# Kernel optimization log

Hardware: AMD Instinct MI355X
Metric: run time of the kernel (lower is better)

Reference implementation:

```python
import jax, jax.numpy as jnp
import numpy as np

B, S, H, NH = 1, 4096, 2048, 16
HD = H // NH
SCALE = HD ** -0.5


def setup_inputs() -> dict:
    key = jax.random.key(0)
    ks = jax.random.split(key, 9)
    std = 1.0 / np.sqrt(H)
    return {
        "hidden_states": jax.random.normal(ks[0], (B, S, H), dtype=jnp.float32),
        "Wq": jax.random.normal(ks[1], (H, H), dtype=jnp.float32) * std,
        "bq": jax.random.normal(ks[2], (H,), dtype=jnp.float32) * std,
        "Wk": jax.random.normal(ks[3], (H, H), dtype=jnp.float32) * std,
        "bk": jax.random.normal(ks[4], (H,), dtype=jnp.float32) * std,
        "Wv": jax.random.normal(ks[5], (H, H), dtype=jnp.float32) * std,
        "bv": jax.random.normal(ks[6], (H,), dtype=jnp.float32) * std,
        "Wo": jax.random.normal(ks[7], (H, H), dtype=jnp.float32) * std,
        "bo": jax.random.normal(ks[8], (H,), dtype=jnp.float32) * std,
    }


def reference(hidden_states, Wq, bq, Wk, bk, Wv, bv, Wo, bo):
    b, s, _ = hidden_states.shape
    # torch nn.Linear: x @ W.T + b
    q = hidden_states @ Wq.T + bq
    k = hidden_states @ Wk.T + bk
    v = hidden_states @ Wv.T + bv
    # [b, nh, s, hd]
    q = q.reshape(b, s, NH, HD).transpose(0, 2, 1, 3)
    k = k.reshape(b, s, NH, HD).transpose(0, 2, 1, 3)
    v = v.reshape(b, s, NH, HD).transpose(0, 2, 1, 3)
    # chunked attention over queries with no mask == full attention
    scores = jnp.einsum('bhqd,bhkd->bhqk', q, k) * SCALE
    attn = jax.nn.softmax(scores, axis=-1)
    out = jnp.einsum('bhqk,bhkd->bhqd', attn, v)
    out = out.transpose(0, 2, 1, 3).reshape(b, s, H)
    return out @ Wo.T + bo
```

## Files before the change

### kernel.cpp

```cpp
#include <hip/hip_runtime.h>
#include <hip/hip_bf16.h>
#include <stdint.h>

#define S_LEN 4096
#define HDIM 2048
#define NHEADS 16
#define HEADDIM 128
#define SCALE_F 0.08838834764831845f
#define MFIX 12.0f

typedef __attribute__((ext_vector_type(8))) short short8;
typedef __attribute__((ext_vector_type(4))) short short4v;
typedef __attribute__((ext_vector_type(4))) float floatx4;
typedef __hip_bfloat16 bf16;

__device__ inline short f2bf(float x) {
  __hip_bfloat16 h = __float2bfloat16(x);
  short s;
  __builtin_memcpy(&s, &h, 2);
  return s;
}

__device__ inline short8 load8_bf16(const float* p) {
  float4 f0 = *(const float4*)p;
  float4 f1 = *(const float4*)(p + 4);
  short8 v;
  v[0] = f2bf(f0.x); v[1] = f2bf(f0.y); v[2] = f2bf(f0.z); v[3] = f2bf(f0.w);
  v[4] = f2bf(f1.x); v[5] = f2bf(f1.y); v[6] = f2bf(f1.z); v[7] = f2bf(f1.w);
  return v;
}
__device__ inline short8 load8_bf16(const bf16* p) { return *(const short8*)p; }

__device__ inline void storeC(bf16* C, size_t idx, float v) { C[idx] = __float2bfloat16(v); }
__device__ inline void storeC(float* C, size_t idx, float v) { C[idx] = v; }

__device__ inline void async_cp16(const void* g, void* l) {
  __builtin_amdgcn_global_load_lds((const __attribute__((address_space(1))) void*)g,
                                   (__attribute__((address_space(3))) void*)l, 16, 0, 0);
}

__global__ __launch_bounds__(256)
void cvt_f32_bf16(const float* __restrict__ in, bf16* __restrict__ out) {
  size_t i = ((size_t)blockIdx.x * 256 + threadIdx.x) * 8;
  *(short8*)((short*)out + i) = load8_bf16(in + i);
}

template<int M, int N, int K, bool TRANSC, bool AASYNC, bool BASYNC,
         typename TA, typename TB, typename TC>
__global__ __launch_bounds__(256, 2)
void gemm_bt(const TA* __restrict__ A, const TB* __restrict__ W,
             const float* __restrict__ bias, TC* __restrict__ C) {
  __shared__ __align__(16) short As[128 * 64];
  __shared__ __align__(16) short Bs[128 * 64];
  const int bn = blockIdx.x * 128;
  const int bm = blockIdx.y * 128;
  const int tid = threadIdx.x;
  const int lane = tid & 63;
  const int wave = tid >> 6;
  const int wr = (wave >> 1) * 64;
  const int wc = (wave & 1) * 64;
  const int ln15 = lane & 15;
  const int quad = lane >> 4;
  const int l8 = lane >> 3;
  const int s8 = lane & 7;
  const int cg = s8 ^ l8;

  floatx4 acc[4][4];
#pragma unroll
  for (int i = 0; i < 4; i++)
#pragma unroll
    for (int j = 0; j < 4; j++) acc[i][j] = floatx4{0.f, 0.f, 0.f, 0.f};

  const TA* Abase = A + (size_t)bm * K;
  const TB* Wbase = W + (size_t)bn * K;

  for (int k0 = 0; k0 < K; k0 += 64) {
#pragma unroll
    for (int is = 0; is < 4; is++) {
      int r = is * 32 + wave * 8 + l8;
      if constexpr (AASYNC)
        async_cp16(Abase + (size_t)r * K + k0 + cg * 8, &As[(is * 32 + wave * 8) * 64]);
      else
        *(short8*)&As[r * 64 + s8 * 8] = load8_bf16(Abase + (size_t)r * K + k0 + cg * 8);
      if constexpr (BASYNC)
        async_cp16(Wbase + (size_t)r * K + k0 + cg * 8, &Bs[(is * 32 + wave * 8) * 64]);
      else
        *(short8*)&Bs[r * 64 + s8 * 8] = load8_bf16(Wbase + (size_t)r * K + k0 + cg * 8);
    }
    __syncthreads();
#pragma unroll
    for (int ks = 0; ks < 2; ks++) {
      short8 af[4], bfr[4];
#pragma unroll
      for (int i = 0; i < 4; i++) {
        int row = wr + i * 16 + ln15;
        af[i] = *(const short8*)&As[row * 64 + (((ks * 4 + quad) ^ (ln15 & 7)) * 8)];
      }
#pragma unroll
      for (int j = 0; j < 4; j++) {
        int row = wc + j * 16 + ln15;
        bfr[j] = *(const short8*)&Bs[row * 64 + (((ks * 4 + quad) ^ (ln15 & 7)) * 8)];
      }
#pragma unroll
      for (int i = 0; i < 4; i++)
#pragma unroll
        for (int j = 0; j < 4; j++)
          acc[i][j] = __builtin_amdgcn_mfma_f32_16x16x32_bf16(af[i], bfr[j], acc[i][j], 0, 0, 0);
    }
    __syncthreads();
  }
#pragma unroll
  for (int j = 0; j < 4; j++) {
    int col = bn + wc + j * 16 + ln15;
    float bv = bias[col];
#pragma unroll
    for (int i = 0; i < 4; i++) {
      int row0 = bm + wr + i * 16 + quad * 4;
      if constexpr (TRANSC) {
        short4v v;
#pragma unroll
        for (int r = 0; r < 4; r++) v[r] = f2bf(acc[i][j][r] + bv);
        *(short4v*)&C[(size_t)col * M + row0] = v;
      } else {
#pragma unroll
        for (int r = 0; r < 4; r++)
          storeC(C, (size_t)(row0 + r) * N + col, acc[i][j][r] + bv);
      }
    }
  }
}

__global__ __launch_bounds__(256, 2)
void flash_attn(const bf16* Qg, const bf16* __restrict__ Kg,
                const bf16* __restrict__ VTg, bf16* Og) {
  __shared__ __align__(16) short Ks[64 * 128];
  __shared__ __align__(16) short Vt[128 * 64];
  __shared__ __align__(16) short Ps[4][32 * 72];

  const int h = blockIdx.x;
  const int q0 = blockIdx.y * 128;
  const int tid = threadIdx.x;
  const int lane = tid & 63;
  const int wave = tid >> 6;
  const int ln15 = lane & 15;
  const int quad = lane >> 4;
  const int l8 = lane >> 3, s8 = lane & 7;
  const int l16 = lane >> 4, s16 = lane & 15;
  const int hoff = h * HEADDIM;
  const int qrow = q0 + wave * 32;

  short8 qf[2][4];
#pragma unroll
  for (int mt = 0; mt < 2; mt++)
#pragma unroll
    for (int ks = 0; ks < 4; ks++)
      qf[mt][ks] = *(const short8*)&Qg[(size_t)(qrow + mt * 16 + ln15) * HDIM + hoff +
                                       ks * 32 + quad * 8];

  floatx4 acc_o[2][8];
#pragma unroll
  for (int mt = 0; mt < 2; mt++)
#pragma unroll
    for (int n = 0; n < 8; n++) acc_o[mt][n] = floatx4{0.f, 0.f, 0.f, 0.f};
  floatx4 l_acc[2] = {floatx4{0.f, 0.f, 0.f, 0.f}, floatx4{0.f, 0.f, 0.f, 0.f}};

  short8 ones;
#pragma unroll
  for (int j = 0; j < 8; j++) ones[j] = (short)0x3F80;

  short* Pw = &Ps[wave][0];

  for (int kv0 = 0; kv0 < S_LEN; kv0 += 64) {
#pragma unroll
    for (int is = 0; is < 4; is++) {
      int r = wave * 16 + is * 4 + l16;
      int cgk = s16 ^ (r & 7);
      async_cp16(&Kg[(size_t)(kv0 + r) * HDIM + hoff + cgk * 8],
                 &Ks[(wave * 16 + is * 4) * 128]);
    }
#pragma unroll
    for (int is = 0; is < 4; is++) {
      int r = wave * 32 + is * 8 + l8;
      async_cp16(&VTg[(size_t)(hoff + r) * S_LEN + kv0 + ((s8 ^ l8) * 8)],
                 &Vt[(wave * 32 + is * 8) * 64]);
    }
    __syncthreads();

    floatx4 sacc[2][4];
#pragma unroll
    for (int mt = 0; mt < 2; mt++)
#pragma unroll
      for (int t = 0; t < 4; t++) sacc[mt][t] = floatx4{0.f, 0.f, 0.f, 0.f};
#pragma unroll
    for (int t = 0; t < 4; t++)
#pragma unroll
      for (int ks = 0; ks < 4; ks++) {
        short8 kf = *(const short8*)&Ks[(t * 16 + ln15) * 128 +
                                        (((ks * 4 + quad) ^ (ln15 & 7)) * 8)];
        sacc[0][t] = __builtin_amdgcn_mfma_f32_16x16x32_bf16(qf[0][ks], kf, sacc[0][t], 0, 0, 0);
        sacc[1][t] = __builtin_amdgcn_mfma_f32_16x16x32_bf16(qf[1][ks], kf, sacc[1][t], 0, 0, 0);
      }

#pragma unroll
    for (int mt = 0; mt < 2; mt++)
#pragma unroll
      for (int t = 0; t < 4; t++)
#pragma unroll
        for (int r = 0; r < 4; r++) {
          float p = __expf(fmaf(sacc[mt][t][r], SCALE_F, -MFIX));
          Pw[(mt * 16 + quad * 4 + r) * 72 + t * 16 + ln15] = f2bf(p);
        }

    short8 pf[2][2];
#pragma unroll
    for (int mt = 0; mt < 2; mt++)
#pragma unroll
      for (int ks = 0; ks < 2; ks++)
        pf[mt][ks] = *(const short8*)&Pw[(mt * 16 + ln15) * 72 + ks * 32 + quad * 8];

#pragma unroll
    for (int mt = 0; mt < 2; mt++)
#pragma unroll
      for (int ks = 0; ks < 2; ks++)
        l_acc[mt] = __builtin_amdgcn_mfma_f32_16x16x32_bf16(pf[mt][ks], ones, l_acc[mt], 0, 0, 0);

#pragma unroll
    for (int n = 0; n < 8; n++)
#pragma unroll
      for (int ks = 0; ks < 2; ks++) {
        short8 vf = *(const short8*)&Vt[(n * 16 + ln15) * 64 +
                                        (((ks * 4 + quad) ^ (ln15 & 7)) * 8)];
        acc_o[0][n] = __builtin_amdgcn_mfma_f32_16x16x32_bf16(pf[0][ks], vf, acc_o[0][n], 0, 0, 0);
        acc_o[1][n] = __builtin_amdgcn_mfma_f32_16x16x32_bf16(pf[1][ks], vf, acc_o[1][n], 0, 0, 0);
      }
    __syncthreads();
  }

#pragma unroll
  for (int mt = 0; mt < 2; mt++) {
    float inv[4];
#pragma unroll
    for (int r = 0; r < 4; r++) inv[r] = 1.0f / l_acc[mt][r];
#pragma unroll
    for (int n = 0; n < 8; n++) {
      int col = hoff + n * 16 + ln15;
#pragma unroll
      for (int r = 0; r < 4; r++) {
        int row = qrow + mt * 16 + quad * 4 + r;
        Og[(size_t)row * HDIM + col] = __float2bfloat16(acc_o[mt][n][r] * inv[r]);
      }
    }
  }
}

extern "C" void kernel_launch(void* const* d_in, const int* in_sizes, int n_in,
                              void* d_out, int out_size, void* d_ws, size_t ws_size,
                              hipStream_t stream) {
  const float* X  = (const float*)d_in[0];
  const float* Wq = (const float*)d_in[1];
  const float* bq = (const float*)d_in[2];
  const float* Wk = (const float*)d_in[3];
  const float* bk = (const float*)d_in[4];
  const float* Wv = (const float*)d_in[5];
  const float* bv = (const float*)d_in[6];
  const float* Wo = (const float*)d_in[7];
  const float* bo = (const float*)d_in[8];
  float* out = (float*)d_out;

  const size_t matS = (size_t)S_LEN * HDIM;
  const size_t matW = (size_t)HDIM * HDIM;
  const size_t need_full = 2 * (matS + matW + 3 * matS);

  dim3 gg(HDIM / 128, S_LEN / 128), bb(256);
  dim3 fg(NHEADS, S_LEN / 128);

  if (ws_size >= need_full) {
    bf16* Xb  = (bf16*)d_ws;
    bf16* Wb  = Xb + matS;
    bf16* Qb  = Wb + matW;
    bf16* Kb  = Qb + matS;
    bf16* VTb = Kb + matS;
    bf16* Ab  = Qb;

    cvt_f32_bf16<<<matS / 2048, 256, 0, stream>>>(X, Xb);
    cvt_f32_bf16<<<matW / 2048, 256, 0, stream>>>(Wq, Wb);
    gemm_bt<S_LEN, HDIM, HDIM, false, true, true, bf16, bf16, bf16>
        <<<gg, bb, 0, stream>>>(Xb, Wb, bq, Qb);
    cvt_f32_bf16<<<matW / 2048, 256, 0, stream>>>(Wk, Wb);
    gemm_bt<S_LEN, HDIM, HDIM, false, true, true, bf16, bf16, bf16>
        <<<gg, bb, 0, stream>>>(Xb, Wb, bk, Kb);
    cvt_f32_bf16<<<matW / 2048, 256, 0, stream>>>(Wv, Wb);
    gemm_bt<S_LEN, HDIM, HDIM, true, true, true, bf16, bf16, bf16>
        <<<gg, bb, 0, stream>>>(Xb, Wb, bv, VTb);

    flash_attn<<<fg, bb, 0, stream>>>(Qb, Kb, VTb, Ab);

    cvt_f32_bf16<<<matW / 2048, 256, 0, stream>>>(Wo, Wb);
    gemm_bt<S_LEN, HDIM, HDIM, false, true, true, bf16, bf16, float>
        <<<gg, bb, 0, stream>>>(Ab, Wb, bo, out);
  } else {
    bf16* Qb  = (bf16*)d_ws;
    bf16* Kb  = Qb + matS;
    bf16* VTb = Kb + matS;
    bf16* Ab  = Qb;

    gemm_bt<S_LEN, HDIM, HDIM, false, false, false, float, float, bf16>
        <<<gg, bb, 0, stream>>>(X, Wq, bq, Qb);
    gemm_bt<S_LEN, HDIM, HDIM, false, false, false, float, float, bf16>
        <<<gg, bb, 0, stream>>>(X, Wk, bk, Kb);
    gemm_bt<S_LEN, HDIM, HDIM, true, false, false, float, float, bf16>
        <<<gg, bb, 0, stream>>>(X, Wv, bv, VTb);

    flash_attn<<<fg, bb, 0, stream>>>(Qb, Kb, VTb, Ab);

    gemm_bt<S_LEN, HDIM, HDIM, false, true, false, bf16, float, float>
        <<<gg, bb, 0, stream>>>(Ab, Wo, bo, out);
  }
}
```

Before: 454.8 us.

## Batch QKV projections into one launch and load V fragments directly from global

The three Q/K/V projection GEMMs are merged into one kernel with a z grid dimension of 3, so they run as a single wider launch. The kernel reads fp32 weights and converts them to bf16 while loading, which removes the separate weight-conversion kernels. Flash attention stops staging V^T in LDS and loads each V fragment straight from global memory into registers, trading LDS traffic and capacity for more global loads and register pressure. The small-workspace fallback path is removed, so the code now assumes the larger workspace is always available.

```diff
diff --git a/kernel.cpp b/kernel.cpp
--- a/kernel.cpp
+++ b/kernel.cpp
@@ -45,10 +45,96 @@
   *(short8*)((short*)out + i) = load8_bf16(in + i);
 }
 
-template<int M, int N, int K, bool TRANSC, bool AASYNC, bool BASYNC,
-         typename TA, typename TB, typename TC>
+__global__ __launch_bounds__(256, 3)
+void gemm_qkv(const bf16* __restrict__ Xb,
+              const float* __restrict__ Wq, const float* __restrict__ Wk,
+              const float* __restrict__ Wv,
+              const float* __restrict__ bq, const float* __restrict__ bk,
+              const float* __restrict__ bv,
+              bf16* __restrict__ Qb, bf16* __restrict__ Kb, bf16* __restrict__ VTb) {
+  constexpr int M = S_LEN, N = HDIM, K = HDIM;
+  __shared__ __align__(16) short As[128 * 64];
+  __shared__ __align__(16) short Bs[128 * 64];
+  const int z = blockIdx.z;
+  const float* W = (z == 0) ? Wq : (z == 1) ? Wk : Wv;
+  const float* bias = (z == 0) ? bq : (z == 1) ? bk : bv;
+  bf16* C = (z == 0) ? Qb : (z == 1) ? Kb : VTb;
+
+  const int bn = blockIdx.x * 128;
+  const int bm = blockIdx.y * 128;
+  const int tid = threadIdx.x;
+  const int lane = tid & 63;
+  const int wave = tid >> 6;
+  const int wr = (wave >> 1) * 64;
+  const int wc = (wave & 1) * 64;
+  const int ln15 = lane & 15;
+  const int quad = lane >> 4;
+  const int l8 = lane >> 3;
+  const int s8 = lane & 7;
+  const int cg = s8 ^ l8;
+
+  floatx4 acc[4][4];
+#pragma unroll
+  for (int i = 0; i < 4; i++)
+#pragma unroll
+    for (int j = 0; j < 4; j++) acc[i][j] = floatx4{0.f, 0.f, 0.f, 0.f};
+
+  const bf16* Abase = Xb + (size_t)bm * K;
+  const float* Wbase = W + (size_t)bn * K;
+
+  for (int k0 = 0; k0 < K; k0 += 64) {
+#pragma unroll
+    for (int is = 0; is < 4; is++) {
+      int r = is * 32 + wave * 8 + l8;
+      async_cp16(Abase + (size_t)r * K + k0 + cg * 8, &As[(is * 32 + wave * 8) * 64]);
+      *(short8*)&Bs[r * 64 + s8 * 8] = load8_bf16(Wbase + (size_t)r * K + k0 + cg * 8);
+    }
+    __syncthreads();
+#pragma unroll
+    for (int ks = 0; ks < 2; ks++) {
+      short8 af[4], bfr[4];
+#pragma unroll
+      for (int i = 0; i < 4; i++) {
+        int row = wr + i * 16 + ln15;
+        af[i] = *(const short8*)&As[row * 64 + (((ks * 4 + quad) ^ (ln15 & 7)) * 8)];
+      }
+#pragma unroll
+      for (int j = 0; j < 4; j++) {
+        int row = wc + j * 16 + ln15;
+        bfr[j] = *(const short8*)&Bs[row * 64 + (((ks * 4 + quad) ^ (ln15 & 7)) * 8)];
+      }
+#pragma unroll
+      for (int i = 0; i < 4; i++)
+#pragma unroll
+        for (int j = 0; j < 4; j++)
+          acc[i][j] = __builtin_amdgcn_mfma_f32_16x16x32_bf16(af[i], bfr[j], acc[i][j], 0, 0, 0);
+    }
+    __syncthreads();
+  }
+#pragma unroll
+  for (int j = 0; j < 4; j++) {
+    int col = bn + wc + j * 16 + ln15;
+    float bv_ = bias[col];
+#pragma unroll
+    for (int i = 0; i < 4; i++) {
+      int row0 = bm + wr + i * 16 + quad * 4;
+      if (z == 2) {
+        short4v v;
+#pragma unroll
+        for (int r = 0; r < 4; r++) v[r] = f2bf(acc[i][j][r] + bv_);
+        *(short4v*)&C[(size_t)col * M + row0] = v;
+      } else {
+#pragma unroll
+        for (int r = 0; r < 4; r++)
+          C[(size_t)(row0 + r) * N + col] = __float2bfloat16(acc[i][j][r] + bv_);
+      }
+    }
+  }
+}
+
+template<int M, int N, int K, typename TC>
 __global__ __launch_bounds__(256, 2)
-void gemm_bt(const TA* __restrict__ A, const TB* __restrict__ W,
+void gemm_bt(const bf16* __restrict__ A, const bf16* __restrict__ W,
              const float* __restrict__ bias, TC* __restrict__ C) {
   __shared__ __align__(16) short As[128 * 64];
   __shared__ __align__(16) short Bs[128 * 64];
@@ -71,21 +157,15 @@
 #pragma unroll
     for (int j = 0; j < 4; j++) acc[i][j] = floatx4{0.f, 0.f, 0.f, 0.f};
 
-  const TA* Abase = A + (size_t)bm * K;
-  const TB* Wbase = W + (size_t)bn * K;
+  const bf16* Abase = A + (size_t)bm * K;
+  const bf16* Wbase = W + (size_t)bn * K;
 
   for (int k0 = 0; k0 < K; k0 += 64) {
 #pragma unroll
     for (int is = 0; is < 4; is++) {
-      int r = is * 32 + wave * 8 + l8;
-      if constexpr (AASYNC)
-        async_cp16(Abase + (size_t)r * K + k0 + cg * 8, &As[(is * 32 + wave * 8) * 64]);
-      else
-        *(short8*)&As[r * 64 + s8 * 8] = load8_bf16(Abase + (size_t)r * K + k0 + cg * 8);
-      if constexpr (BASYNC)
-        async_cp16(Wbase + (size_t)r * K + k0 + cg * 8, &Bs[(is * 32 + wave * 8) * 64]);
-      else
-        *(short8*)&Bs[r * 64 + s8 * 8] = load8_bf16(Wbase + (size_t)r * K + k0 + cg * 8);
+      int r = is * 32 + wave * 8;
+      async_cp16(Abase + (size_t)(r + l8) * K + k0 + cg * 8, &As[r * 64]);
+      async_cp16(Wbase + (size_t)(r + l8) * K + k0 + cg * 8, &Bs[r * 64]);
     }
     __syncthreads();
 #pragma unroll
@@ -112,20 +192,13 @@
 #pragma unroll
   for (int j = 0; j < 4; j++) {
     int col = bn + wc + j * 16 + ln15;
-    float bv = bias[col];
+    float bv_ = bias[col];
 #pragma unroll
     for (int i = 0; i < 4; i++) {
       int row0 = bm + wr + i * 16 + quad * 4;
-      if constexpr (TRANSC) {
-        short4v v;
-#pragma unroll
-        for (int r = 0; r < 4; r++) v[r] = f2bf(acc[i][j][r] + bv);
-        *(short4v*)&C[(size_t)col * M + row0] = v;
-      } else {
-#pragma unroll
-        for (int r = 0; r < 4; r++)
-          storeC(C, (size_t)(row0 + r) * N + col, acc[i][j][r] + bv);
-      }
+#pragma unroll
+      for (int r = 0; r < 4; r++)
+        storeC(C, (size_t)(row0 + r) * N + col, acc[i][j][r] + bv_);
     }
   }
 }
@@ -134,7 +207,6 @@
 void flash_attn(const bf16* Qg, const bf16* __restrict__ Kg,
                 const bf16* __restrict__ VTg, bf16* Og) {
   __shared__ __align__(16) short Ks[64 * 128];
-  __shared__ __align__(16) short Vt[128 * 64];
   __shared__ __align__(16) short Ps[4][32 * 72];
 
   const int h = blockIdx.x;
@@ -144,7 +216,6 @@
   const int wave = tid >> 6;
   const int ln15 = lane & 15;
   const int quad = lane >> 4;
-  const int l8 = lane >> 3, s8 = lane & 7;
   const int l16 = lane >> 4, s16 = lane & 15;
   const int hoff = h * HEADDIM;
   const int qrow = q0 + wave * 32;
@@ -169,6 +240,7 @@
   for (int j = 0; j < 8; j++) ones[j] = (short)0x3F80;
 
   short* Pw = &Ps[wave][0];
+  const bf16* vbase = VTg + (size_t)(hoff + ln15) * S_LEN + quad * 8;
 
   for (int kv0 = 0; kv0 < S_LEN; kv0 += 64) {
 #pragma unroll
@@ -178,13 +250,14 @@
       async_cp16(&Kg[(size_t)(kv0 + r) * HDIM + hoff + cgk * 8],
                  &Ks[(wave * 16 + is * 4) * 128]);
     }
-#pragma unroll
-    for (int is = 0; is < 4; is++) {
-      int r = wave * 32 + is * 8 + l8;
-      async_cp16(&VTg[(size_t)(hoff + r) * S_LEN + kv0 + ((s8 ^ l8) * 8)],
-                 &Vt[(wave * 32 + is * 8) * 64]);
-    }
-    __syncthreads();
+    __syncthreads();
+
+    short8 vf[8][2];
+#pragma unroll
+    for (int n = 0; n < 8; n++)
+#pragma unroll
+      for (int ks = 0; ks < 2; ks++)
+        vf[n][ks] = *(const short8*)&vbase[(size_t)(n * 16) * S_LEN + kv0 + ks * 32];
 
     floatx4 sacc[2][4];
 #pragma unroll
@@ -228,10 +301,8 @@
     for (int n = 0; n < 8; n++)
 #pragma unroll
       for (int ks = 0; ks < 2; ks++) {
-        short8 vf = *(const short8*)&Vt[(n * 16 + ln15) * 64 +
-                                        (((ks * 4 + quad) ^ (ln15 & 7)) * 8)];
-        acc_o[0][n] = __builtin_amdgcn_mfma_f32_16x16x32_bf16(pf[0][ks], vf, acc_o[0][n], 0, 0, 0);
-        acc_o[1][n] = __builtin_amdgcn_mfma_f32_16x16x32_bf16(pf[1][ks], vf, acc_o[1][n], 0, 0, 0);
+        acc_o[0][n] = __builtin_amdgcn_mfma_f32_16x16x32_bf16(pf[0][ks], vf[n][ks], acc_o[0][n], 0, 0, 0);
+        acc_o[1][n] = __builtin_amdgcn_mfma_f32_16x16x32_bf16(pf[1][ks], vf[n][ks], acc_o[1][n], 0, 0, 0);
       }
     __syncthreads();
   }
@@ -269,51 +340,22 @@
 
   const size_t matS = (size_t)S_LEN * HDIM;
   const size_t matW = (size_t)HDIM * HDIM;
-  const size_t need_full = 2 * (matS + matW + 3 * matS);
-
-  dim3 gg(HDIM / 128, S_LEN / 128), bb(256);
-  dim3 fg(NHEADS, S_LEN / 128);
-
-  if (ws_size >= need_full) {
-    bf16* Xb  = (bf16*)d_ws;
-    bf16* Wb  = Xb + matS;
-    bf16* Qb  = Wb + matW;
-    bf16* Kb  = Qb + matS;
-    bf16* VTb = Kb + matS;
-    bf16* Ab  = Qb;
-
-    cvt_f32_bf16<<<matS / 2048, 256, 0, stream>>>(X, Xb);
-    cvt_f32_bf16<<<matW / 2048, 256, 0, stream>>>(Wq, Wb);
-    gemm_bt<S_LEN, HDIM, HDIM, false, true, true, bf16, bf16, bf16>
-        <<<gg, bb, 0, stream>>>(Xb, Wb, bq, Qb);
-    cvt_f32_bf16<<<matW / 2048, 256, 0, stream>>>(Wk, Wb);
-    gemm_bt<S_LEN, HDIM, HDIM, false, true, true, bf16, bf16, bf16>
-        <<<gg, bb, 0, stream>>>(Xb, Wb, bk, Kb);
-    cvt_f32_bf16<<<matW / 2048, 256, 0, stream>>>(Wv, Wb);
-    gemm_bt<S_LEN, HDIM, HDIM, true, true, true, bf16, bf16, bf16>
-        <<<gg, bb, 0, stream>>>(Xb, Wb, bv, VTb);
-
-    flash_attn<<<fg, bb, 0, stream>>>(Qb, Kb, VTb, Ab);
-
-    cvt_f32_bf16<<<matW / 2048, 256, 0, stream>>>(Wo, Wb);
-    gemm_bt<S_LEN, HDIM, HDIM, false, true, true, bf16, bf16, float>
-        <<<gg, bb, 0, stream>>>(Ab, Wb, bo, out);
-  } else {
-    bf16* Qb  = (bf16*)d_ws;
-    bf16* Kb  = Qb + matS;
-    bf16* VTb = Kb + matS;
-    bf16* Ab  = Qb;
-
-    gemm_bt<S_LEN, HDIM, HDIM, false, false, false, float, float, bf16>
-        <<<gg, bb, 0, stream>>>(X, Wq, bq, Qb);
-    gemm_bt<S_LEN, HDIM, HDIM, false, false, false, float, float, bf16>
-        <<<gg, bb, 0, stream>>>(X, Wk, bk, Kb);
-    gemm_bt<S_LEN, HDIM, HDIM, true, false, false, float, float, bf16>
-        <<<gg, bb, 0, stream>>>(X, Wv, bv, VTb);
-
-    flash_attn<<<fg, bb, 0, stream>>>(Qb, Kb, VTb, Ab);
-
-    gemm_bt<S_LEN, HDIM, HDIM, false, true, false, bf16, float, float>
-        <<<gg, bb, 0, stream>>>(Ab, Wo, bo, out);
-  }
-}
+
+  bf16* Xb  = (bf16*)d_ws;
+  bf16* Qb  = Xb + matS;
+  bf16* Kb  = Qb + matS;
+  bf16* VTb = Kb + matS;
+  bf16* Wb  = VTb + matS;
+  bf16* Ab  = Qb;
+
+  cvt_f32_bf16<<<matS / 2048, 256, 0, stream>>>(X, Xb);
+  cvt_f32_bf16<<<matW / 2048, 256, 0, stream>>>(Wo, Wb);
+
+  gemm_qkv<<<dim3(HDIM / 128, S_LEN / 128, 3), 256, 0, stream>>>(
+      Xb, Wq, Wk, Wv, bq, bk, bv, Qb, Kb, VTb);
+
+  flash_attn<<<dim3(NHEADS, S_LEN / 128), 256, 0, stream>>>(Qb, Kb, VTb, Ab);
+
+  gemm_bt<S_LEN, HDIM, HDIM, float>
+      <<<dim3(HDIM / 128, S_LEN / 128), 256, 0, stream>>>(Ab, Wb, bo, out);
+}
```

Measured after the change: 689.3 us. 1.52x slower.
